# Optimization experiments

Measured on AMD Instinct MI355X. Metric: run time of the kernel, lower is better.

## Reference

```python
import jax, jax.numpy as jnp
import numpy as np

B, IN, H = 4096, 1024, 1024


def setup_inputs() -> dict:
    key = jax.random.key(0)
    ks = jax.random.split(key, 20)
    s_in = 1.0 / np.sqrt(IN)
    s_h = 1.0 / np.sqrt(H)
    def lin(kw, kb, fan_in, scale):
        W = jax.random.uniform(kw, (H, fan_in), jnp.float32, -scale, scale)
        b = jax.random.uniform(kb, (H,), jnp.float32, -scale, scale)
        return W, b
    Wxf, bxf = lin(ks[0], ks[1], IN, s_in)
    Whf, bhf = lin(ks[2], ks[3], H, s_h)
    Wxi, bxi = lin(ks[4], ks[5], IN, s_in)
    Whi, bhi = lin(ks[6], ks[7], H, s_h)
    Wxo, bxo = lin(ks[8], ks[9], IN, s_in)
    Who, bho = lin(ks[10], ks[11], H, s_h)
    Wxc, bxc = lin(ks[12], ks[13], IN, s_in)
    Whc, bhc = lin(ks[14], ks[15], H, s_h)
    x = jax.random.normal(ks[16], (B, IN), jnp.float32)
    c = jax.random.normal(ks[17], (B, H), jnp.float32)
    h = jax.random.normal(ks[18], (B, H), jnp.float32)
    return dict(x=x, c=c, h=h,
                Wxf=Wxf, bxf=bxf, Whf=Whf, bhf=bhf,
                Wxi=Wxi, bxi=bxi, Whi=Whi, bhi=bhi,
                Wxo=Wxo, bxo=bxo, Who=Who, bho=bho,
                Wxc=Wxc, bxc=bxc, Whc=Whc, bhc=bhc)


def reference(x, c, h,
              Wxf, bxf, Whf, bhf,
              Wxi, bxi, Whi, bhi,
              Wxo, bxo, Who, bho,
              Wxc, bxc, Whc, bhc):
    # Fuse the 8 small GEMMs into two batched GEMMs: x @ Wx^T and h @ Wh^T
    # with gate outputs concatenated along the hidden dim [f, i, o, c~].
    Wx = jnp.concatenate([Wxf, Wxi, Wxo, Wxc], axis=0)   # [4H, IN]
    Wh = jnp.concatenate([Whf, Whi, Who, Whc], axis=0)   # [4H, H]
    bx = jnp.concatenate([bxf, bxi, bxo, bxc], axis=0)   # [4H]
    bh = jnp.concatenate([bhf, bhi, bho, bhc], axis=0)   # [4H]
    gates = x @ Wx.T + h @ Wh.T + (bx + bh)              # [B, 4H]
    hs = Wxf.shape[0]
    f = jax.nn.sigmoid(gates[:, 0 * hs:1 * hs])
    i = jax.nn.sigmoid(gates[:, 1 * hs:2 * hs])
    o = jax.nn.sigmoid(gates[:, 2 * hs:3 * hs])
    ctil = jnp.tanh(gates[:, 3 * hs:4 * hs])
    ct = f * c + ctil * i
    ht = jnp.tanh(ct) * o
    return (ct, ht)
```

## Files before the change

### kernel.cpp

```cpp
#include <hip/hip_runtime.h>
#include <hip/hip_bf16.h>
#include <stdint.h>

typedef __hip_bfloat16 bf16;
typedef __attribute__((ext_vector_type(8))) short short8;
typedef __attribute__((ext_vector_type(4))) float floatx4;

#define AS1(p) ((const __attribute__((address_space(1))) void*)(p))
#define AS3(p) ((__attribute__((address_space(3))) void*)(p))

#define M_DIM 4096
#define H_DIM 1024
#define MEG   (1u << 20)
#define LDS_BUF 24576

__device__ __forceinline__ unsigned short f2bf(float f) {
    uint32_t u = __float_as_uint(f);
    uint32_t r = (u + 0x7FFFu + ((u >> 16) & 1u)) >> 16;
    return (unsigned short)r;
}

__device__ __forceinline__ float fast_sigmoid(float v) {
    return 1.0f / (1.0f + __expf(-v));
}
__device__ __forceinline__ float fast_tanh(float v) {
    return 2.0f / (1.0f + __expf(-2.0f * v)) - 1.0f;
}

__global__ __launch_bounds__(256)
void pack_bf16(const float* __restrict__ x, const float* __restrict__ h,
               const float* Wxf, const float* Wxi, const float* Wxo, const float* Wxc,
               const float* Whf, const float* Whi, const float* Who, const float* Whc,
               unsigned short* __restrict__ ws)
{
    const int w = threadIdx.x >> 6;
    const int l = threadIdx.x & 63;
    const uint32_t W = blockIdx.x * 4u + (uint32_t)w;

    const uint32_t r  = (uint32_t)l >> 2;
    const uint32_t kg = ((uint32_t)l & 3u) ^ ((r >> 1) & 3u);

    const float* src;
    uint32_t row, kt;
    if (W < 16384u) {
        const uint32_t Wa = W & 8191u;
        const uint32_t ch = Wa & 7u;
        kt = (Wa >> 3) & 31u;
        const uint32_t mx = Wa >> 8;
        src = (W < 8192u) ? x : h;
        row = mx * 128u + ch * 16u + r;
    } else {
        const uint32_t V = W & 8191u;
        kt = V & 31u;
        uint32_t U = V >> 5;
        const uint32_t b4 = U & 3u;
        const uint32_t g  = (U >> 2) & 3u;
        const uint32_t ny = U >> 4;
        if (W < 24576u)
            src = (g == 0) ? Wxf : (g == 1) ? Wxi : (g == 2) ? Wxo : Wxc;
        else
            src = (g == 0) ? Whf : (g == 1) ? Whi : (g == 2) ? Who : Whc;
        row = ny * 64u + b4 * 16u + r;
    }
    const float* s = src + (size_t)row * 1024u + kt * 32u + kg * 8u;
    const float4 v0 = *(const float4*)s;
    const float4 v1 = *(const float4*)(s + 4);
    short8 pk;
    pk[0] = (short)f2bf(v0.x); pk[1] = (short)f2bf(v0.y);
    pk[2] = (short)f2bf(v0.z); pk[3] = (short)f2bf(v0.w);
    pk[4] = (short)f2bf(v1.x); pk[5] = (short)f2bf(v1.y);
    pk[6] = (short)f2bf(v1.z); pk[7] = (short)f2bf(v1.w);
    *(short8*)(ws + (size_t)W * 512u + (uint32_t)l * 8u) = pk;
}

__global__ __launch_bounds__(512, 4)
void lstm_fused_kernel(const unsigned short* __restrict__ ws,
                       const float* __restrict__ c,
                       const float* __restrict__ bxf, const float* __restrict__ bhf,
                       const float* __restrict__ bxi, const float* __restrict__ bhi,
                       const float* __restrict__ bxo, const float* __restrict__ bho,
                       const float* __restrict__ bxc, const float* __restrict__ bhc,
                       float* __restrict__ out)
{
    __shared__ __align__(16) char lds[3 * LDS_BUF];

    const int tid  = threadIdx.x;
    const int w    = tid >> 6;
    const int lane = tid & 63;

    const int bid = blockIdx.x;
    const int mx  = bid >> 4;
    const int ny  = ((bid & 7) << 1) | ((bid >> 3) & 1);
    const int bm0 = mx * 128;
    const int bn0 = ny * 64;

    const unsigned short* srcP0[3];
    const unsigned short* srcP1[3];
    uint32_t kstr[3];
    uint32_t loff[3];
#pragma unroll
    for (int i = 0; i < 3; ++i) {
        const int ch = w * 3 + i;
        if (ch < 8) {
            const uint32_t base = ((uint32_t)mx * 32u * 8u + (uint32_t)ch) * 512u;
            srcP0[i] = ws + base + (uint32_t)lane * 8u;
            srcP1[i] = srcP0[i] + (8u << 20);
            kstr[i]  = 8u * 512u;
            loff[i]  = (uint32_t)ch * 1024u;
        } else {
            const int b  = ch - 8;
            const uint32_t g  = (uint32_t)b >> 2;
            const uint32_t b4 = (uint32_t)b & 3u;
            const uint32_t base = (16384u + ((uint32_t)ny * 16u + g * 4u + b4) * 32u) * 512u;
            srcP0[i] = ws + base + (uint32_t)lane * 8u;
            srcP1[i] = srcP0[i] + (8192u * 512u);
            kstr[i]  = 512u;
            loff[i]  = 8192u + (uint32_t)b * 1024u;
        }
    }
#pragma unroll
    for (int i = 0; i < 3; ++i) {
        const int ch = w * 3 + i;
        if (ch < 8) srcP1[i] = srcP0[i] + 8192u * 512u;
    }

    const int wrow  = (w & 1) * 64;
    const int wcol  = (w >> 1) * 16;
    const int lrc   = lane & 15;
    const int lquad = lane >> 4;

    const uint32_t kslot = (((uint32_t)lquad ^ (((uint32_t)lrc >> 1) & 3u))) * 8u;

    uint32_t aoff[4];
#pragma unroll
    for (int mt = 0; mt < 4; ++mt)
        aoff[mt] = (uint32_t)((wrow + mt * 16 + lrc) * 32) + kslot;
    uint32_t boff[4];
#pragma unroll
    for (int g = 0; g < 4; ++g)
        boff[g] = (uint32_t)(g * 2048 + (wcol + lrc) * 32) + kslot;

    floatx4 acc[4][4];
#pragma unroll
    for (int g = 0; g < 4; ++g)
#pragma unroll
        for (int mt = 0; mt < 4; ++mt)
            acc[g][mt] = (floatx4){0.f, 0.f, 0.f, 0.f};

    auto issue_loads = [&](int kt, uint32_t stage) {
        const int phase = kt >> 5;
        const uint32_t kk = (uint32_t)(kt & 31);
        const uint32_t bb = stage * LDS_BUF;
#pragma unroll
        for (int i = 0; i < 3; ++i) {
            const unsigned short* src = (phase ? srcP1[i] : srcP0[i]) + kk * kstr[i];
            __builtin_amdgcn_global_load_lds(AS1(src), AS3(lds + bb + loff[i]), 16, 0, 0);
        }
    };
    auto compute = [&](uint32_t stage) {
        const char* base = lds + stage * LDS_BUF;
        const bf16* lA = (const bf16*)base;
        const bf16* lB = (const bf16*)(base + 8192);
        short8 afr[4];
#pragma unroll
        for (int mt = 0; mt < 4; ++mt)
            afr[mt] = *(const short8*)(lA + aoff[mt]);
#pragma unroll
        for (int g = 0; g < 4; ++g) {
            const short8 bfr = *(const short8*)(lB + boff[g]);
#pragma unroll
            for (int mt = 0; mt < 4; ++mt)
                acc[g][mt] = __builtin_amdgcn_mfma_f32_16x16x32_bf16(
                    afr[mt], bfr, acc[g][mt], 0, 0, 0);
        }
    };

    issue_loads(0, 0);
    issue_loads(1, 1);

    uint32_t s_comp = 0;
    uint32_t s_load = 2;
    for (int kt = 0; kt < 62; ++kt) {
        asm volatile("s_waitcnt vmcnt(3)\ns_barrier" ::: "memory");
        issue_loads(kt + 2, s_load);
        compute(s_comp);
        s_comp = (s_comp == 2) ? 0 : s_comp + 1;
        s_load = (s_load == 2) ? 0 : s_load + 1;
    }
    asm volatile("s_waitcnt vmcnt(3)\ns_barrier" ::: "memory");
    compute(s_comp);
    s_comp = (s_comp == 2) ? 0 : s_comp + 1;
    asm volatile("s_waitcnt vmcnt(0)\ns_barrier" ::: "memory");
    compute(s_comp);

    float* out_ct = out;
    float* out_ht = out + (size_t)M_DIM * H_DIM;
    {
        const int col = bn0 + wcol + lrc;
        const float bf_ = bxf[col] + bhf[col];
        const float bi_ = bxi[col] + bhi[col];
        const float bo_ = bxo[col] + bho[col];
        const float bc_ = bxc[col] + bhc[col];
#pragma unroll
        for (int mt = 0; mt < 4; ++mt) {
#pragma unroll
            for (int r = 0; r < 4; ++r) {
                const int row = bm0 + wrow + mt * 16 + lquad * 4 + r;
                const float gf = acc[0][mt][r] + bf_;
                const float gi = acc[1][mt][r] + bi_;
                const float go = acc[2][mt][r] + bo_;
                const float gc = acc[3][mt][r] + bc_;
                const float f    = fast_sigmoid(gf);
                const float ii   = fast_sigmoid(gi);
                const float o    = fast_sigmoid(go);
                const float ctil = fast_tanh(gc);
                const float cv   = c[(size_t)row * H_DIM + col];
                const float ctn  = f * cv + ctil * ii;
                const float htn  = fast_tanh(ctn) * o;
                out_ct[(size_t)row * H_DIM + col] = ctn;
                out_ht[(size_t)row * H_DIM + col] = htn;
            }
        }
    }
}

extern "C" void kernel_launch(void* const* d_in, const int* in_sizes, int n_in,
                              void* d_out, int out_size, void* d_ws, size_t ws_size,
                              hipStream_t stream) {
    (void)in_sizes; (void)n_in; (void)out_size; (void)ws_size;
    const float* x   = (const float*)d_in[0];
    const float* c   = (const float*)d_in[1];
    const float* h   = (const float*)d_in[2];
    const float* Wxf = (const float*)d_in[3];  const float* bxf = (const float*)d_in[4];
    const float* Whf = (const float*)d_in[5];  const float* bhf = (const float*)d_in[6];
    const float* Wxi = (const float*)d_in[7];  const float* bxi = (const float*)d_in[8];
    const float* Whi = (const float*)d_in[9];  const float* bhi = (const float*)d_in[10];
    const float* Wxo = (const float*)d_in[11]; const float* bxo = (const float*)d_in[12];
    const float* Who = (const float*)d_in[13]; const float* bho = (const float*)d_in[14];
    const float* Wxc = (const float*)d_in[15]; const float* bxc = (const float*)d_in[16];
    const float* Whc = (const float*)d_in[17]; const float* bhc = (const float*)d_in[18];
    float* out = (float*)d_out;
    unsigned short* ws = (unsigned short*)d_ws;

    pack_bf16<<<8192, 256, 0, stream>>>(x, h,
        Wxf, Wxi, Wxo, Wxc, Whf, Whi, Who, Whc, ws);

    lstm_fused_kernel<<<512, 512, 0, stream>>>(ws, c,
        bxf, bhf, bxi, bhi, bxo, bho, bxc, bhc, out);
}
```

Baseline: 213.9 us.

## Double M-tile to 256, add 4-stage LDS pipeline with split MFMA phases

Enlarges each workgroup's output tile from 128x64 to 256x64, so each wave holds 8x4 accumulators and the grid halves to 256 blocks. The pack kernel is re-laid out so x/h and Wx/Wh tiles for all 64 k-steps are contiguous per tile. The main loop gets a 4-stage LDS ring with loads issued in two halves, interleaved with two MFMA batches separated by barriers, s_setprio boosts, and an XCD-aware block remap. This aims to raise arithmetic intensity and overlap global loads with MFMA. It also raises register and LDS pressure, drops occupancy, and leaves 256 blocks, which may underfill the CUs.

```diff
diff --git a/kernel.cpp b/kernel.cpp
--- a/kernel.cpp
+++ b/kernel.cpp
@@ -11,8 +11,7 @@
 
 #define M_DIM 4096
 #define H_DIM 1024
-#define MEG   (1u << 20)
-#define LDS_BUF 24576
+#define STAGE_BYTES 32768
 
 __device__ __forceinline__ unsigned short f2bf(float f) {
     uint32_t u = __float_as_uint(f);
@@ -41,28 +40,30 @@
     const uint32_t kg = ((uint32_t)l & 3u) ^ ((r >> 1) & 3u);
 
     const float* src;
-    uint32_t row, kt;
+    uint32_t row, ktl;
     if (W < 16384u) {
-        const uint32_t Wa = W & 8191u;
-        const uint32_t ch = Wa & 7u;
-        kt = (Wa >> 3) & 31u;
-        const uint32_t mx = Wa >> 8;
-        src = (W < 8192u) ? x : h;
-        row = mx * 128u + ch * 16u + r;
+        const uint32_t ch = W & 15u;
+        const uint32_t KT = (W >> 4) & 63u;
+        const uint32_t mx = W >> 10;
+        src = (KT < 32u) ? x : h;
+        ktl = KT & 31u;
+        row = mx * 256u + ch * 16u + r;
     } else {
-        const uint32_t V = W & 8191u;
-        kt = V & 31u;
-        uint32_t U = V >> 5;
-        const uint32_t b4 = U & 3u;
-        const uint32_t g  = (U >> 2) & 3u;
+        const uint32_t V  = W & 16383u;
+        const uint32_t KT = V & 63u;
+        const uint32_t U  = V >> 6;
+        const uint32_t b  = U & 15u;
         const uint32_t ny = U >> 4;
-        if (W < 24576u)
+        const uint32_t g  = b >> 2;
+        const uint32_t c4 = b & 3u;
+        if (KT < 32u)
             src = (g == 0) ? Wxf : (g == 1) ? Wxi : (g == 2) ? Wxo : Wxc;
         else
             src = (g == 0) ? Whf : (g == 1) ? Whi : (g == 2) ? Who : Whc;
-        row = ny * 64u + b4 * 16u + r;
-    }
-    const float* s = src + (size_t)row * 1024u + kt * 32u + kg * 8u;
+        ktl = KT & 31u;
+        row = ny * 64u + c4 * 16u + r;
+    }
+    const float* s = src + (size_t)row * 1024u + ktl * 32u + kg * 8u;
     const float4 v0 = *(const float4*)s;
     const float4 v1 = *(const float4*)(s + 4);
     short8 pk;
@@ -73,7 +74,55 @@
     *(short8*)(ws + (size_t)W * 512u + (uint32_t)l * 8u) = pk;
 }
 
-__global__ __launch_bounds__(512, 4)
+#define GLL(srcp, dstp) __builtin_amdgcn_global_load_lds(AS1(srcp), AS3(dstp), 16, 0, 0)
+
+#define VMW8 asm volatile("s_waitcnt vmcnt(8)" ::: "memory")
+#define VMW4 asm volatile("s_waitcnt vmcnt(4)" ::: "memory")
+#define VMW0 asm volatile("s_waitcnt vmcnt(0)" ::: "memory")
+#define VMNONE ((void)0)
+
+#define ITER(kt_, ISSUE_, VMA_)                                                   \
+  {                                                                               \
+    const uint32_t sc_ = (uint32_t)(kt_) & 3u;                                    \
+    const uint32_t sl_ = (uint32_t)((kt_) + 3) & 3u;                              \
+    const bf16* base_ = (const bf16*)(lds + sc_ * STAGE_BYTES);                   \
+    char* ldst_ = lds + sl_ * STAGE_BYTES;                                        \
+    short8 bfr_[4], afr_[4];                                                      \
+    _Pragma("unroll") for (int g_ = 0; g_ < 4; ++g_)                              \
+        bfr_[g_] = *(const short8*)(base_ + boff[g_]);                            \
+    _Pragma("unroll") for (int m_ = 0; m_ < 4; ++m_)                              \
+        afr_[m_] = *(const short8*)(base_ + aoff[m_]);                            \
+    if (ISSUE_) { GLL(srcP[0] + ko0, ldst_ + loffA[0]);                           \
+                  GLL(srcP[1] + ko1, ldst_ + loffA[1]); }                         \
+    __builtin_amdgcn_s_barrier();                                                 \
+    asm volatile("s_waitcnt lgkmcnt(0)" ::: "memory");                            \
+    __builtin_amdgcn_sched_barrier(0);                                            \
+    __builtin_amdgcn_s_setprio(1);                                                \
+    _Pragma("unroll") for (int g_ = 0; g_ < 4; ++g_)                              \
+      _Pragma("unroll") for (int m_ = 0; m_ < 4; ++m_)                            \
+        acc[g_][m_] = __builtin_amdgcn_mfma_f32_16x16x32_bf16(                    \
+            afr_[m_], bfr_[g_], acc[g_][m_], 0, 0, 0);                            \
+    __builtin_amdgcn_s_setprio(0);                                                \
+    __builtin_amdgcn_s_barrier();                                                 \
+    _Pragma("unroll") for (int m_ = 0; m_ < 4; ++m_)                              \
+        afr_[m_] = *(const short8*)(base_ + aoff[4 + m_]);                        \
+    if (ISSUE_) { GLL(srcP[2] + ko2, ldst_ + loffA[2]);                           \
+                  GLL(srcP[3] + ko3, ldst_ + loffA[3]);                           \
+                  ko0 += kstr0; ko1 += kstr1; ko2 += kstr2; ko3 += kstr3; }       \
+    VMA_;                                                                         \
+    __builtin_amdgcn_s_barrier();                                                 \
+    asm volatile("s_waitcnt lgkmcnt(0)" ::: "memory");                            \
+    __builtin_amdgcn_sched_barrier(0);                                            \
+    __builtin_amdgcn_s_setprio(1);                                                \
+    _Pragma("unroll") for (int g_ = 0; g_ < 4; ++g_)                              \
+      _Pragma("unroll") for (int m_ = 0; m_ < 4; ++m_)                            \
+        acc[g_][4 + m_] = __builtin_amdgcn_mfma_f32_16x16x32_bf16(                \
+            afr_[m_], bfr_[g_], acc[g_][4 + m_], 0, 0, 0);                        \
+    __builtin_amdgcn_s_setprio(0);                                                \
+    __builtin_amdgcn_s_barrier();                                                 \
+  }
+
+__global__ __launch_bounds__(512, 2)
 void lstm_fused_kernel(const unsigned short* __restrict__ ws,
                        const float* __restrict__ c,
                        const float* __restrict__ bxf, const float* __restrict__ bhf,
@@ -82,116 +131,78 @@
                        const float* __restrict__ bxc, const float* __restrict__ bhc,
                        float* __restrict__ out)
 {
-    __shared__ __align__(16) char lds[3 * LDS_BUF];
+    __shared__ __align__(16) char lds[4 * STAGE_BYTES];
 
     const int tid  = threadIdx.x;
     const int w    = tid >> 6;
     const int lane = tid & 63;
 
-    const int bid = blockIdx.x;
-    const int mx  = bid >> 4;
-    const int ny  = ((bid & 7) << 1) | ((bid >> 3) & 1);
-    const int bm0 = mx * 128;
+    const int bid  = blockIdx.x;
+    const int wgid = (bid & 7) * 32 + (bid >> 3);
+    const int mx  = wgid >> 4;
+    const int ny  = wgid & 15;
+    const int bm0 = mx * 256;
     const int bn0 = ny * 64;
 
-    const unsigned short* srcP0[3];
-    const unsigned short* srcP1[3];
-    uint32_t kstr[3];
-    uint32_t loff[3];
-#pragma unroll
-    for (int i = 0; i < 3; ++i) {
-        const int ch = w * 3 + i;
-        if (ch < 8) {
-            const uint32_t base = ((uint32_t)mx * 32u * 8u + (uint32_t)ch) * 512u;
-            srcP0[i] = ws + base + (uint32_t)lane * 8u;
-            srcP1[i] = srcP0[i] + (8u << 20);
-            kstr[i]  = 8u * 512u;
-            loff[i]  = (uint32_t)ch * 1024u;
+    const unsigned short* srcP[4];
+    uint32_t loffA[4];
+    uint32_t kstr0, kstr1, kstr2, kstr3;
+    uint32_t ks_[4];
+#pragma unroll
+    for (int i = 0; i < 4; ++i) {
+        const int ch = w * 4 + i;
+        if (ch < 16) {
+            srcP[i]  = ws + ((uint32_t)mx * 1024u + (uint32_t)ch) * 512u
+                          + (uint32_t)lane * 8u;
+            ks_[i]   = 16u * 512u;
+            loffA[i] = (uint32_t)ch * 1024u;
         } else {
-            const int b  = ch - 8;
-            const uint32_t g  = (uint32_t)b >> 2;
-            const uint32_t b4 = (uint32_t)b & 3u;
-            const uint32_t base = (16384u + ((uint32_t)ny * 16u + g * 4u + b4) * 32u) * 512u;
-            srcP0[i] = ws + base + (uint32_t)lane * 8u;
-            srcP1[i] = srcP0[i] + (8192u * 512u);
-            kstr[i]  = 512u;
-            loff[i]  = 8192u + (uint32_t)b * 1024u;
+            const int b = ch - 16;
+            srcP[i]  = ws + (16384u + ((uint32_t)ny * 16u + (uint32_t)b) * 64u) * 512u
+                          + (uint32_t)lane * 8u;
+            ks_[i]   = 512u;
+            loffA[i] = 16384u + (uint32_t)b * 1024u;
         }
     }
-#pragma unroll
-    for (int i = 0; i < 3; ++i) {
-        const int ch = w * 3 + i;
-        if (ch < 8) srcP1[i] = srcP0[i] + 8192u * 512u;
-    }
-
-    const int wrow  = (w & 1) * 64;
+    kstr0 = ks_[0]; kstr1 = ks_[1]; kstr2 = ks_[2]; kstr3 = ks_[3];
+
+    const int wrow  = (w & 1) * 128;
     const int wcol  = (w >> 1) * 16;
     const int lrc   = lane & 15;
     const int lquad = lane >> 4;
 
-    const uint32_t kslot = (((uint32_t)lquad ^ (((uint32_t)lrc >> 1) & 3u))) * 8u;
-
-    uint32_t aoff[4];
-#pragma unroll
-    for (int mt = 0; mt < 4; ++mt)
-        aoff[mt] = (uint32_t)((wrow + mt * 16 + lrc) * 32) + kslot;
+    const uint32_t kslot = ((uint32_t)lquad ^ (((uint32_t)lrc >> 1) & 3u)) * 8u;
+
+    uint32_t aoff[8];
+#pragma unroll
+    for (int mt = 0; mt < 8; ++mt)
+        aoff[mt] = (uint32_t)(((wrow >> 4) + mt) * 512) + (uint32_t)lrc * 32u + kslot;
     uint32_t boff[4];
 #pragma unroll
     for (int g = 0; g < 4; ++g)
-        boff[g] = (uint32_t)(g * 2048 + (wcol + lrc) * 32) + kslot;
-
-    floatx4 acc[4][4];
+        boff[g] = 8192u + (uint32_t)((g * 4 + (w >> 1)) * 512) + (uint32_t)lrc * 32u + kslot;
+
+    floatx4 acc[4][8];
 #pragma unroll
     for (int g = 0; g < 4; ++g)
 #pragma unroll
-        for (int mt = 0; mt < 4; ++mt)
+        for (int mt = 0; mt < 8; ++mt)
             acc[g][mt] = (floatx4){0.f, 0.f, 0.f, 0.f};
 
-    auto issue_loads = [&](int kt, uint32_t stage) {
-        const int phase = kt >> 5;
-        const uint32_t kk = (uint32_t)(kt & 31);
-        const uint32_t bb = stage * LDS_BUF;
-#pragma unroll
-        for (int i = 0; i < 3; ++i) {
-            const unsigned short* src = (phase ? srcP1[i] : srcP0[i]) + kk * kstr[i];
-            __builtin_amdgcn_global_load_lds(AS1(src), AS3(lds + bb + loff[i]), 16, 0, 0);
-        }
-    };
-    auto compute = [&](uint32_t stage) {
-        const char* base = lds + stage * LDS_BUF;
-        const bf16* lA = (const bf16*)base;
-        const bf16* lB = (const bf16*)(base + 8192);
-        short8 afr[4];
-#pragma unroll
-        for (int mt = 0; mt < 4; ++mt)
-            afr[mt] = *(const short8*)(lA + aoff[mt]);
-#pragma unroll
-        for (int g = 0; g < 4; ++g) {
-            const short8 bfr = *(const short8*)(lB + boff[g]);
-#pragma unroll
-            for (int mt = 0; mt < 4; ++mt)
-                acc[g][mt] = __builtin_amdgcn_mfma_f32_16x16x32_bf16(
-                    afr[mt], bfr, acc[g][mt], 0, 0, 0);
-        }
-    };
-
-    issue_loads(0, 0);
-    issue_loads(1, 1);
-
-    uint32_t s_comp = 0;
-    uint32_t s_load = 2;
-    for (int kt = 0; kt < 62; ++kt) {
-        asm volatile("s_waitcnt vmcnt(3)\ns_barrier" ::: "memory");
-        issue_loads(kt + 2, s_load);
-        compute(s_comp);
-        s_comp = (s_comp == 2) ? 0 : s_comp + 1;
-        s_load = (s_load == 2) ? 0 : s_load + 1;
-    }
-    asm volatile("s_waitcnt vmcnt(3)\ns_barrier" ::: "memory");
-    compute(s_comp);
-    s_comp = (s_comp == 2) ? 0 : s_comp + 1;
-    asm volatile("s_waitcnt vmcnt(0)\ns_barrier" ::: "memory");
-    compute(s_comp);
+#pragma unroll
+    for (int t = 0; t < 3; ++t) {
+#pragma unroll
+        for (int i = 0; i < 4; ++i)
+            GLL(srcP[i] + (uint32_t)t * ks_[i], lds + t * STAGE_BYTES + loffA[i]);
+    }
+    uint32_t ko0 = 3u * kstr0, ko1 = 3u * kstr1, ko2 = 3u * kstr2, ko3 = 3u * kstr3;
+    VMW8;
+    __builtin_amdgcn_s_barrier();
+
+    for (int kt = 0; kt < 61; ++kt) ITER(kt, 1, VMW8);
+    ITER(61, 0, VMW4);
+    ITER(62, 0, VMW0);
+    ITER(63, 0, VMNONE);
 
     float* out_ct = out;
     float* out_ht = out + (size_t)M_DIM * H_DIM;
@@ -202,7 +213,7 @@
         const float bo_ = bxo[col] + bho[col];
         const float bc_ = bxc[col] + bhc[col];
 #pragma unroll
-        for (int mt = 0; mt < 4; ++mt) {
+        for (int mt = 0; mt < 8; ++mt) {
 #pragma unroll
             for (int r = 0; r < 4; ++r) {
                 const int row = bm0 + wrow + mt * 16 + lquad * 4 + r;
@@ -245,6 +256,6 @@
     pack_bf16<<<8192, 256, 0, stream>>>(x, h,
         Wxf, Wxi, Wxo, Wxc, Whf, Whi, Who, Whc, ws);
 
-    lstm_fused_kernel<<<512, 512, 0, stream>>>(ws, c,
+    lstm_fused_kernel<<<256, 512, 0, stream>>>(ws, c,
         bxf, bhf, bxi, bhi, bxo, bho, bxc, bhc, out);
 }
```

Result: no change. 216.2 us (+1.1%).

## Switch to 32x32x16 MFMA with repacked K-major layout and LDS gate exchange

Applied to the files above, without the earlier changes.

Replaces the 16x16x32 bf16 MFMA tiling with 32x32x16 MFMAs, each wave computing two 32x32 tiles across two gates. The pack kernel is relaid so each 16-byte lane load maps directly to a 32-row by 16-K fragment, and the main loop is manually unrolled by three stages with macro-based issue and compute. Because each wave now holds only two gates, the epilogue exchanges activated gate values between paired waves through LDS before forming c_t and h_t. The aim is fewer LDS fragment reads and instructions per MFMA FLOP, at the cost of an extra LDS round-trip and barriers in the epilogue.

```diff
diff --git a/kernel.cpp b/kernel.cpp
--- a/kernel.cpp
+++ b/kernel.cpp
@@ -4,22 +4,20 @@
 
 typedef __hip_bfloat16 bf16;
 typedef __attribute__((ext_vector_type(8))) short short8;
-typedef __attribute__((ext_vector_type(4))) float floatx4;
+typedef __attribute__((ext_vector_type(16))) float floatx16;
 
 #define AS1(p) ((const __attribute__((address_space(1))) void*)(p))
 #define AS3(p) ((__attribute__((address_space(3))) void*)(p))
 
 #define M_DIM 4096
 #define H_DIM 1024
-#define MEG   (1u << 20)
-#define LDS_BUF 24576
+#define STAGE 24576
 
 __device__ __forceinline__ unsigned short f2bf(float f) {
     uint32_t u = __float_as_uint(f);
     uint32_t r = (u + 0x7FFFu + ((u >> 16) & 1u)) >> 16;
     return (unsigned short)r;
 }
-
 __device__ __forceinline__ float fast_sigmoid(float v) {
     return 1.0f / (1.0f + __expf(-v));
 }
@@ -37,32 +35,32 @@
     const int l = threadIdx.x & 63;
     const uint32_t W = blockIdx.x * 4u + (uint32_t)w;
 
-    const uint32_t r  = (uint32_t)l >> 2;
-    const uint32_t kg = ((uint32_t)l & 3u) ^ ((r >> 1) & 3u);
+    const uint32_t r  = (uint32_t)l & 31u;
+    const uint32_t kh = (uint32_t)l >> 5;
 
     const float* src;
-    uint32_t row, kt;
+    uint32_t row, kq;
     if (W < 16384u) {
-        const uint32_t Wa = W & 8191u;
-        const uint32_t ch = Wa & 7u;
-        kt = (Wa >> 3) & 31u;
-        const uint32_t mx = Wa >> 8;
-        src = (W < 8192u) ? x : h;
-        row = mx * 128u + ch * 16u + r;
+        const uint32_t ch4 = W & 3u;
+        kq = (W >> 2) & 127u;
+        const uint32_t mx = W >> 9;
+        src = (kq < 64u) ? x : h;
+        row = mx * 128u + ch4 * 32u + r;
     } else {
-        const uint32_t V = W & 8191u;
-        kt = V & 31u;
-        uint32_t U = V >> 5;
-        const uint32_t b4 = U & 3u;
-        const uint32_t g  = (U >> 2) & 3u;
-        const uint32_t ny = U >> 4;
-        if (W < 24576u)
+        const uint32_t V  = W - 16384u;
+        kq = V & 127u;
+        const uint32_t U  = V >> 7;
+        const uint32_t b8 = U & 7u;
+        const uint32_t ny = U >> 3;
+        const uint32_t g  = b8 >> 1;
+        const uint32_t nh = b8 & 1u;
+        if (kq < 64u)
             src = (g == 0) ? Wxf : (g == 1) ? Wxi : (g == 2) ? Wxo : Wxc;
         else
             src = (g == 0) ? Whf : (g == 1) ? Whi : (g == 2) ? Who : Whc;
-        row = ny * 64u + b4 * 16u + r;
-    }
-    const float* s = src + (size_t)row * 1024u + kt * 32u + kg * 8u;
+        row = ny * 64u + nh * 32u + r;
+    }
+    const float* s = src + (size_t)row * 1024u + (kq & 63u) * 16u + kh * 8u;
     const float4 v0 = *(const float4*)s;
     const float4 v1 = *(const float4*)(s + 4);
     short8 pk;
@@ -72,6 +70,41 @@
     pk[6] = (short)f2bf(v1.z); pk[7] = (short)f2bf(v1.w);
     *(short8*)(ws + (size_t)W * 512u + (uint32_t)l * 8u) = pk;
 }
+
+#define GLL(srcp, dstp) __builtin_amdgcn_global_load_lds(AS1(srcp), AS3(dstp), 16, 0, 0)
+#define WAITB(N) do {                                                         \
+    asm volatile("s_waitcnt vmcnt(" #N ") lgkmcnt(0)\ns_barrier" ::: "memory");\
+    __builtin_amdgcn_sched_barrier(0);                                        \
+} while (0)
+
+#define MFMA32(a, b, c) __builtin_amdgcn_mfma_f32_32x32x16_bf16((a), (b), (c), 0, 0, 0)
+
+#define ISSUE(SL) do {                                                        \
+    GLL(p0, lds + (SL)*STAGE + loff0); p0 += ks0;                             \
+    GLL(p1, lds + (SL)*STAGE + loff1); p1 += ks1;                             \
+    GLL(p2, lds + (SL)*STAGE + loff2); p2 += ks2;                             \
+} while (0)
+
+#define COMPUTE(SC) do {                                                      \
+    short8 a0_ = *(const short8*)(ldsA + (SC)*STAGE + 0);                     \
+    short8 a1_ = *(const short8*)(ldsA + (SC)*STAGE + 1024);                  \
+    short8 b0_ = *(const short8*)(ldsB + (SC)*STAGE + 0);                     \
+    short8 b1_ = *(const short8*)(ldsB + (SC)*STAGE + 2048);                  \
+    acc00 = MFMA32(a0_, b0_, acc00);                                          \
+    acc01 = MFMA32(a1_, b0_, acc01);                                          \
+    acc10 = MFMA32(a0_, b1_, acc10);                                          \
+    acc11 = MFMA32(a1_, b1_, acc11);                                          \
+    a0_ = *(const short8*)(ldsA + (SC)*STAGE + 4096);                         \
+    a1_ = *(const short8*)(ldsA + (SC)*STAGE + 4096 + 1024);                  \
+    b0_ = *(const short8*)(ldsB + (SC)*STAGE + 8192);                         \
+    b1_ = *(const short8*)(ldsB + (SC)*STAGE + 8192 + 2048);                  \
+    acc00 = MFMA32(a0_, b0_, acc00);                                          \
+    acc01 = MFMA32(a1_, b0_, acc01);                                          \
+    acc10 = MFMA32(a0_, b1_, acc10);                                          \
+    acc11 = MFMA32(a1_, b1_, acc11);                                          \
+} while (0)
+
+#define ITER(SC, SL) do { WAITB(3); ISSUE(SL); COMPUTE(SC); } while (0)
 
 __global__ __launch_bounds__(512, 4)
 void lstm_fused_kernel(const unsigned short* __restrict__ ws,
@@ -82,7 +115,7 @@
                        const float* __restrict__ bxc, const float* __restrict__ bhc,
                        float* __restrict__ out)
 {
-    __shared__ __align__(16) char lds[3 * LDS_BUF];
+    __shared__ __align__(16) char lds[3 * STAGE];
 
     const int tid  = threadIdx.x;
     const int w    = tid >> 6;
@@ -94,131 +127,128 @@
     const int bm0 = mx * 128;
     const int bn0 = ny * 64;
 
-    const unsigned short* srcP0[3];
-    const unsigned short* srcP1[3];
-    uint32_t kstr[3];
-    uint32_t loff[3];
-#pragma unroll
-    for (int i = 0; i < 3; ++i) {
-        const int ch = w * 3 + i;
-        if (ch < 8) {
-            const uint32_t base = ((uint32_t)mx * 32u * 8u + (uint32_t)ch) * 512u;
-            srcP0[i] = ws + base + (uint32_t)lane * 8u;
-            srcP1[i] = srcP0[i] + (8u << 20);
-            kstr[i]  = 8u * 512u;
-            loff[i]  = (uint32_t)ch * 1024u;
-        } else {
-            const int b  = ch - 8;
-            const uint32_t g  = (uint32_t)b >> 2;
-            const uint32_t b4 = (uint32_t)b & 3u;
-            const uint32_t base = (16384u + ((uint32_t)ny * 16u + g * 4u + b4) * 32u) * 512u;
-            srcP0[i] = ws + base + (uint32_t)lane * 8u;
-            srcP1[i] = srcP0[i] + (8192u * 512u);
-            kstr[i]  = 512u;
-            loff[i]  = 8192u + (uint32_t)b * 1024u;
-        }
-    }
-#pragma unroll
-    for (int i = 0; i < 3; ++i) {
-        const int ch = w * 3 + i;
-        if (ch < 8) srcP1[i] = srcP0[i] + 8192u * 512u;
-    }
-
-    const int wrow  = (w & 1) * 64;
-    const int wcol  = (w >> 1) * 16;
-    const int lrc   = lane & 15;
-    const int lquad = lane >> 4;
-
-    const uint32_t kslot = (((uint32_t)lquad ^ (((uint32_t)lrc >> 1) & 3u))) * 8u;
-
-    uint32_t aoff[4];
-#pragma unroll
-    for (int mt = 0; mt < 4; ++mt)
-        aoff[mt] = (uint32_t)((wrow + mt * 16 + lrc) * 32) + kslot;
-    uint32_t boff[4];
-#pragma unroll
-    for (int g = 0; g < 4; ++g)
-        boff[g] = (uint32_t)(g * 2048 + (wcol + lrc) * 32) + kslot;
-
-    floatx4 acc[4][4];
-#pragma unroll
-    for (int g = 0; g < 4; ++g)
-#pragma unroll
-        for (int mt = 0; mt < 4; ++mt)
-            acc[g][mt] = (floatx4){0.f, 0.f, 0.f, 0.f};
-
-    auto issue_loads = [&](int kt, uint32_t stage) {
-        const int phase = kt >> 5;
-        const uint32_t kk = (uint32_t)(kt & 31);
-        const uint32_t bb = stage * LDS_BUF;
-#pragma unroll
-        for (int i = 0; i < 3; ++i) {
-            const unsigned short* src = (phase ? srcP1[i] : srcP0[i]) + kk * kstr[i];
-            __builtin_amdgcn_global_load_lds(AS1(src), AS3(lds + bb + loff[i]), 16, 0, 0);
-        }
-    };
-    auto compute = [&](uint32_t stage) {
-        const char* base = lds + stage * LDS_BUF;
-        const bf16* lA = (const bf16*)base;
-        const bf16* lB = (const bf16*)(base + 8192);
-        short8 afr[4];
-#pragma unroll
-        for (int mt = 0; mt < 4; ++mt)
-            afr[mt] = *(const short8*)(lA + aoff[mt]);
-#pragma unroll
-        for (int g = 0; g < 4; ++g) {
-            const short8 bfr = *(const short8*)(lB + boff[g]);
-#pragma unroll
-            for (int mt = 0; mt < 4; ++mt)
-                acc[g][mt] = __builtin_amdgcn_mfma_f32_16x16x32_bf16(
-                    afr[mt], bfr, acc[g][mt], 0, 0, 0);
-        }
-    };
-
-    issue_loads(0, 0);
-    issue_loads(1, 1);
-
-    uint32_t s_comp = 0;
-    uint32_t s_load = 2;
-    for (int kt = 0; kt < 62; ++kt) {
-        asm volatile("s_waitcnt vmcnt(3)\ns_barrier" ::: "memory");
-        issue_loads(kt + 2, s_load);
-        compute(s_comp);
-        s_comp = (s_comp == 2) ? 0 : s_comp + 1;
-        s_load = (s_load == 2) ? 0 : s_load + 1;
-    }
-    asm volatile("s_waitcnt vmcnt(3)\ns_barrier" ::: "memory");
-    compute(s_comp);
-    s_comp = (s_comp == 2) ? 0 : s_comp + 1;
-    asm volatile("s_waitcnt vmcnt(0)\ns_barrier" ::: "memory");
-    compute(s_comp);
-
+    const int wM = w >> 2;
+    const int wN = (w >> 1) & 1;
+    const int gp = w & 1;
+
+    const unsigned short* p0; const unsigned short* p1; const unsigned short* p2;
+    uint32_t loff0, loff1, loff2, ks0, ks1, ks2;
+#define CHDEC(CH, P, LO, KS) do {                                             \
+    const int ch_ = (CH);                                                     \
+    if (ch_ < 8) {                                                            \
+        const uint32_t kc_ = (uint32_t)ch_ >> 2, c4_ = (uint32_t)ch_ & 3u;    \
+        P = ws + ((uint32_t)mx * 512u + kc_ * 4u + c4_) * 512u                \
+               + (uint32_t)lane * 8u;                                         \
+        KS = 4096u;                                                           \
+    } else {                                                                  \
+        const uint32_t b_ = (uint32_t)(ch_ - 8), kc_ = b_ >> 3, b8_ = b_ & 7u;\
+        P = ws + (16384u + ((uint32_t)ny * 8u + b8_) * 128u + kc_) * 512u     \
+               + (uint32_t)lane * 8u;                                         \
+        KS = 1024u;                                                           \
+    }                                                                         \
+    LO = (uint32_t)ch_ * 1024u;                                               \
+} while (0)
+    CHDEC(w * 3 + 0, p0, loff0, ks0);
+    CHDEC(w * 3 + 1, p1, loff1, ks1);
+    CHDEC(w * 3 + 2, p2, loff2, ks2);
+#undef CHDEC
+
+    const char* ldsA = lds + (uint32_t)lane * 16u + (uint32_t)wM * 2048u;
+    const char* ldsB = lds + (uint32_t)lane * 16u + 8192u
+                           + ((uint32_t)(4 * gp + wN)) * 1024u;
+
+    floatx16 acc00 = {0}, acc01 = {0}, acc10 = {0}, acc11 = {0};
+
+    ISSUE(0);
+    ISSUE(1);
+
+    for (int t = 0; t < 20; ++t) {
+        ITER(0, 2); ITER(1, 0); ITER(2, 1);
+    }
+    ITER(0, 2);
+    ITER(1, 0);
+    WAITB(3); COMPUTE(2);
+    WAITB(0); COMPUTE(0);
+
+    const int colg = bn0 + (wN * 32) + (lane & 31);
+    const int lq   = lane >> 5;
+    const int wrow = wM * 64;
     float* out_ct = out;
     float* out_ht = out + (size_t)M_DIM * H_DIM;
+
+    float bA, bB;
+    if (gp == 0) { bA = bxf[colg] + bhf[colg]; bB = bxi[colg] + bhi[colg]; }
+    else         { bA = bxo[colg] + bho[colg]; bB = bxc[colg] + bhc[colg]; }
+
+    if (gp == 0) {
+#pragma unroll
+        for (int r = 0; r < 16; ++r) {
+            acc00[r] = fast_sigmoid(acc00[r] + bA);
+            acc01[r] = fast_sigmoid(acc01[r] + bA);
+            acc10[r] = fast_sigmoid(acc10[r] + bB);
+            acc11[r] = fast_sigmoid(acc11[r] + bB);
+        }
+    } else {
+#pragma unroll
+        for (int r = 0; r < 16; ++r) {
+            acc00[r] = fast_sigmoid(acc00[r] + bA);
+            acc01[r] = fast_sigmoid(acc01[r] + bA);
+            acc10[r] = fast_tanh(acc10[r] + bB);
+            acc11[r] = fast_tanh(acc11[r] + bB);
+        }
+    }
+
+    __syncthreads();
+
     {
-        const int col = bn0 + wcol + lrc;
-        const float bf_ = bxf[col] + bhf[col];
-        const float bi_ = bxi[col] + bhi[col];
-        const float bo_ = bxo[col] + bho[col];
-        const float bc_ = bxc[col] + bhc[col];
-#pragma unroll
-        for (int mt = 0; mt < 4; ++mt) {
-#pragma unroll
-            for (int r = 0; r < 4; ++r) {
-                const int row = bm0 + wrow + mt * 16 + lquad * 4 + r;
-                const float gf = acc[0][mt][r] + bf_;
-                const float gi = acc[1][mt][r] + bi_;
-                const float go = acc[2][mt][r] + bo_;
-                const float gc = acc[3][mt][r] + bc_;
-                const float f    = fast_sigmoid(gf);
-                const float ii   = fast_sigmoid(gi);
-                const float o    = fast_sigmoid(go);
-                const float ctil = fast_tanh(gc);
-                const float cv   = c[(size_t)row * H_DIM + col];
-                const float ctn  = f * cv + ctil * ii;
-                const float htn  = fast_tanh(ctn) * o;
-                out_ct[(size_t)row * H_DIM + col] = ctn;
-                out_ht[(size_t)row * H_DIM + col] = htn;
+        char* wr = (char*)lds + (uint32_t)(w >> 1) * 16384u + (uint32_t)gp * 8192u;
+        if (gp == 0) {
+#pragma unroll
+            for (int r = 0; r < 16; ++r) {
+                const int ri = (r & 3) + 8 * (r >> 2) + 4 * lq;
+                *(float*)(wr +        ri * 128 + (lane & 31) * 4) = acc01[r];
+                *(float*)(wr + 4096 + ri * 128 + (lane & 31) * 4) = acc11[r];
+            }
+        } else {
+#pragma unroll
+            for (int r = 0; r < 16; ++r) {
+                const int ri = (r & 3) + 8 * (r >> 2) + 4 * lq;
+                *(float*)(wr +        ri * 128 + (lane & 31) * 4) = acc00[r];
+                *(float*)(wr + 4096 + ri * 128 + (lane & 31) * 4) = acc10[r];
+            }
+        }
+    }
+
+    __syncthreads();
+
+    {
+        const char* rd = (const char*)lds + (uint32_t)(w >> 1) * 16384u
+                                          + (uint32_t)(1 - gp) * 8192u;
+        if (gp == 0) {
+#pragma unroll
+            for (int r = 0; r < 16; ++r) {
+                const int ri = (r & 3) + 8 * (r >> 2) + 4 * lq;
+                const float O  = *(const float*)(rd +        ri * 128 + (lane & 31) * 4);
+                const float CT = *(const float*)(rd + 4096 + ri * 128 + (lane & 31) * 4);
+                const int row = bm0 + wrow + ri;
+                const float cv  = c[(size_t)row * H_DIM + colg];
+                const float ctn = acc00[r] * cv + CT * acc10[r];
+                const float htn = fast_tanh(ctn) * O;
+                out_ct[(size_t)row * H_DIM + colg] = ctn;
+                out_ht[(size_t)row * H_DIM + colg] = htn;
+            }
+        } else {
+#pragma unroll
+            for (int r = 0; r < 16; ++r) {
+                const int ri = (r & 3) + 8 * (r >> 2) + 4 * lq;
+                const float F = *(const float*)(rd +        ri * 128 + (lane & 31) * 4);
+                const float I = *(const float*)(rd + 4096 + ri * 128 + (lane & 31) * 4);
+                const int row = bm0 + wrow + 32 + ri;
+                const float cv  = c[(size_t)row * H_DIM + colg];
+                const float ctn = F * cv + acc11[r] * I;
+                const float htn = fast_tanh(ctn) * acc01[r];
+                out_ct[(size_t)row * H_DIM + colg] = ctn;
+                out_ht[(size_t)row * H_DIM + colg] = htn;
             }
         }
     }
```

After: 247.5 us. 1.16x slower.
